# Optimization experiments

Measured on AMD Instinct MI355X. Metric: run time of the kernel, lower is better.

The kernel has to match this reference:

```python
import jax, jax.numpy as jnp
import numpy as np
import math

L, D, H, HD, F, G, V, P = 15, 512, 64, 8, 2048, 128, 7, 49
B, N = 4, 256


def setup_inputs() -> dict:
    key = jax.random.key(0)
    ks = jax.random.split(key, 24)
    nrm = lambda k, shape, s=0.02: (jax.random.normal(k, shape) * s).astype(jnp.float32)
    inp = {}
    inp["atom_types"] = jax.random.randint(ks[0], (B, N), 0, V)
    inp["coords"] = jax.random.normal(ks[1], (B, N, 3)) * 3.0
    inp["pair_types"] = jax.random.randint(ks[2], (B, N, N), 0, P)
    inp["mask"] = jnp.ones((B, N), dtype=bool)
    # embeddings / pair encoding params
    inp["atom_emb"] = nrm(ks[3], (V, D), 1.0).at[0].set(0.0)  # padding_idx=0
    inp["gaussian_mu"] = jax.random.normal(ks[4], (G,))
    inp["gaussian_sigma"] = jnp.ones((G,)) * 0.1
    inp["pair_a"] = jax.random.normal(ks[5], (P,)) * 0.01
    inp["pair_b"] = jax.random.normal(ks[6], (P,)) * 0.01
    inp["pl_w"] = nrm(ks[7], (G,))
    inp["pl_b"] = jnp.zeros(())
    # stacked per-layer params (leading dim L for lax.scan)
    inp["ln1_g"] = jnp.ones((L, D)); inp["ln1_b"] = jnp.zeros((L, D))
    inp["qkv_w"] = nrm(ks[8], (L, 3 * D, D)); inp["qkv_b"] = jnp.zeros((L, 3 * D))
    inp["pp_w"] = nrm(ks[9], (L, H), 0.1); inp["pp_b"] = jnp.zeros((L, H))
    inp["out_w"] = nrm(ks[10], (L, D, D)); inp["out_b"] = jnp.zeros((L, D))
    inp["ln2_g"] = jnp.ones((L, D)); inp["ln2_b"] = jnp.zeros((L, D))
    inp["ffn_w1"] = nrm(ks[11], (L, F, D)); inp["ffn_b1"] = jnp.zeros((L, F))
    inp["ffn_w2"] = nrm(ks[12], (L, D, F)); inp["ffn_b2"] = jnp.zeros((L, D))
    # SE3 head scalar affines (Linear(1,1) twice) and energy head
    inp["se3_uw"] = jnp.array(0.5); inp["se3_ub"] = jnp.array(0.01)
    inp["se3_ww"] = jnp.array(0.5); inp["se3_wb"] = jnp.array(0.01)
    inp["en_w"] = nrm(ks[13], (D,)); inp["en_b"] = jnp.zeros(())
    return inp


def _layernorm(x, g, b):
    m = x.mean(-1, keepdims=True)
    v = ((x - m) ** 2).mean(-1, keepdims=True)
    return (x - m) / jnp.sqrt(v + 1e-5) * g + b


def reference(atom_types, coords, pair_types, mask,
              atom_emb, gaussian_mu, gaussian_sigma, pair_a, pair_b, pl_w, pl_b,
              ln1_g, ln1_b, qkv_w, qkv_b, pp_w, pp_b, out_w, out_b,
              ln2_g, ln2_b, ffn_w1, ffn_b1, ffn_w2, ffn_b2,
              se3_uw, se3_ub, se3_ww, se3_wb, en_w, en_b):
    b_, n_ = atom_types.shape
    h = atom_emb[atom_types]  # [B,N,D]

    delta = coords[:, :, None, :] - coords[:, None, :, :]  # [B,N,N,3]
    d2 = (delta ** 2).sum(-1)
    dist = jnp.sqrt(jnp.maximum(d2, 1e-12))  # safe norm (grad-safe at 0)
    dist = jnp.where(mask[:, :, None], dist, 0.0)
    da = (pair_a[pair_types] * dist + pair_b[pair_types])[..., None]  # [B,N,N,1]
    gt = jnp.exp(-(da - gaussian_mu) ** 2) / (2.0 * gaussian_sigma ** 2)
    gt = gt / (gaussian_sigma * math.sqrt(2.0 * math.pi))
    gt = gt * mask[:, :, None, None]  # [B,N,N,G]
    pair_repr = gt @ pl_w + pl_b  # [B,N,N]
    pair_mask = mask[:, :, None] & mask[:, None, :]
    pair_repr = pair_repr * pair_mask

    scale = 1.0 / math.sqrt(HD)
    row_mask = mask[:, None, :, None]  # masks query rows, per original code

    def layer(hc, p):
        (l1g, l1b, qw, qb, ppw, ppb, ow, ob, l2g, l2b, w1, b1, w2, b2) = p
        x = _layernorm(hc, l1g, l1b)
        qkv = (x @ qw.T + qb).reshape(b_, n_, 3, H, HD)
        q, k, v = qkv[:, :, 0], qkv[:, :, 1], qkv[:, :, 2]
        scores = jnp.einsum('bnhd,bmhd->bhnm', q, k) * scale
        bias = pair_repr[..., None] * ppw + ppb  # [B,N,N,H]
        scores = scores + bias.transpose(0, 3, 1, 2)
        scores = jnp.where(row_mask, scores, -1e9)
        probs = jax.nn.softmax(scores, axis=-1)
        probs = jnp.where(jnp.isnan(probs), 0.0, probs)
        attn = jnp.einsum('bhnm,bmhd->bnhd', probs, v).reshape(b_, n_, D)
        hc = hc + attn @ ow.T + ob
        x2 = _layernorm(hc, l2g, l2b)
        ffn = jax.nn.gelu(x2 @ w1.T + b1, approximate=False) @ w2.T + b2
        return hc + ffn, None

    h, _ = jax.lax.scan(layer, h, (ln1_g, ln1_b, qkv_w, qkv_b, pp_w, pp_b,
                                   out_w, out_b, ln2_g, ln2_b,
                                   ffn_w1, ffn_b1, ffn_w2, ffn_b2))

    # --- SE3 equivariant head ---
    c = jax.nn.relu(pair_repr)[..., None]  # [B,N,N,1]
    c = c * se3_uw + se3_ub
    c = c * se3_ww + se3_wb
    c = c * mask[:, :, None, None]
    update = (delta * c).sum(axis=2)  # [B,N,3]
    num_valid = mask.sum(-1).astype(coords.dtype)[:, None, None] + 1e-6
    pred_coords = coords + update / num_valid

    cls = h[:, 0, :]
    pred_energy = cls @ en_w + en_b  # [B]
    return pred_coords, pred_energy


if __name__ == '__main__':
    out = reference(**setup_inputs())
    print(out[0].shape, out[1].shape)
```

## Files before the change

kernel.cpp:

```cpp
#include <hip/hip_runtime.h>
#include <hip/hip_bf16.h>
#include <math.h>

#define LAY 15
#define DIM 512
#define NH 64
#define HD 8
#define FF 2048
#define NG 128
#define BATCH 4
#define NTOK 256
#define PSTRIDE 524288

typedef __attribute__((ext_vector_type(8))) short short8;
typedef __attribute__((ext_vector_type(4))) short short4v;
typedef __attribute__((ext_vector_type(8))) __bf16 bf16x8;
typedef __attribute__((ext_vector_type(4))) float f32x4;

__device__ inline short f2bs(float f) {
  __bf16 b = (__bf16)f;
  return __builtin_bit_cast(short, b);
}

__global__ __launch_bounds__(256) void embed_kernel(
    const int* __restrict__ types, const float* __restrict__ emb,
    float* __restrict__ h)
{
  int idx = blockIdx.x * 256 + threadIdx.x;
  int token = idx >> 9;
  int d = idx & 511;
  h[idx] = emb[types[token] * DIM + d];
}

__global__ __launch_bounds__(256) void cvt2_kernel(
    const float* __restrict__ qkvw, const float* __restrict__ outw,
    const float* __restrict__ w1, const float* __restrict__ w2,
    short* __restrict__ dst, int basePair)
{
  size_t i = ((size_t)basePair + blockIdx.x * 256 + threadIdx.x) * 2;
  const float* src; size_t off;
  if (i < 1474560)      { src = qkvw; off = i; }
  else if (i < 1966080) { src = outw; off = i - 1474560; }
  else if (i < 3932160) { src = w1;   off = i - 1966080; }
  else                  { src = w2;   off = i - 3932160; }
  const float4* sp = (const float4*)(src + off * 8);
  float4 a = sp[0], b = sp[1], c = sp[2], d = sp[3];
  bf16x8 v0, v1;
  v0[0] = (__bf16)a.x; v0[1] = (__bf16)a.y; v0[2] = (__bf16)a.z; v0[3] = (__bf16)a.w;
  v0[4] = (__bf16)b.x; v0[5] = (__bf16)b.y; v0[6] = (__bf16)b.z; v0[7] = (__bf16)b.w;
  v1[0] = (__bf16)c.x; v1[1] = (__bf16)c.y; v1[2] = (__bf16)c.z; v1[3] = (__bf16)c.w;
  v1[4] = (__bf16)d.x; v1[5] = (__bf16)d.y; v1[6] = (__bf16)d.z; v1[7] = (__bf16)d.w;
  *(short8*)(dst + i * 8) = __builtin_bit_cast(short8, v0);
  *(short8*)(dst + i * 8 + 8) = __builtin_bit_cast(short8, v1);
}

__global__ __launch_bounds__(256) void pair_kernel(
    const int* __restrict__ pair_types, const float* __restrict__ coords,
    const float* __restrict__ mu, const float* __restrict__ sigma,
    const float* __restrict__ pa, const float* __restrict__ pb,
    const float* __restrict__ plw, const float* __restrict__ plb,
    float* __restrict__ pair_repr)
{
  __shared__ float smu[NG], sw[NG];
  int tid = threadIdx.x;
  if (tid < NG) {
    float sg = sigma[tid];
    smu[tid] = mu[tid];
    sw[tid] = plw[tid] / (2.0f * sg * sg * sg * 2.5066282746310002f);
  }
  __syncthreads();
  int idx = blockIdx.x * 256 + tid;
  int b = idx >> 16;
  int ij = idx & 65535;
  int i = ij >> 8, j = ij & 255;
  const float* ci = coords + (b * NTOK + i) * 3;
  const float* cj = coords + (b * NTOK + j) * 3;
  float dx = ci[0] - cj[0], dy = ci[1] - cj[1], dz = ci[2] - cj[2];
  float d2 = dx * dx + dy * dy + dz * dz;
  float dist = sqrtf(fmaxf(d2, 1e-12f));
  int pt = pair_types[idx];
  float da = pa[pt] * dist + pb[pt];
  float acc = 0.0f;
#pragma unroll 8
  for (int g = 0; g < NG; ++g) {
    float t = da - smu[g];
    acc += __expf(-t * t) * sw[g];
  }
  pair_repr[idx] = acc + plb[0];
}

__global__ __launch_bounds__(256) void pairT_kernel(
    const float* __restrict__ pr, float* __restrict__ prT)
{
  __shared__ float tile[32][33];
  int b = blockIdx.z;
  int i0 = blockIdx.y * 32, j0 = blockIdx.x * 32;
  int tx = threadIdx.x & 31, ty = threadIdx.x >> 5;
#pragma unroll
  for (int r = 0; r < 4; ++r)
    tile[ty + r * 8][tx] = pr[((size_t)(b * NTOK + i0 + ty + r * 8)) * NTOK + j0 + tx];
  __syncthreads();
#pragma unroll
  for (int r = 0; r < 4; ++r)
    prT[((size_t)(b * NTOK + j0 + ty + r * 8)) * NTOK + i0 + tx] = tile[tx][ty + r * 8];
}

__global__ __launch_bounds__(256) void coord_kernel(
    const float* __restrict__ coords, const float* __restrict__ pair_repr,
    const float* __restrict__ uw, const float* __restrict__ ub,
    const float* __restrict__ ww, const float* __restrict__ wb,
    float* __restrict__ out)
{
  int bi = blockIdx.x;
  int b = bi >> 8;
  int j = threadIdx.x;
  float pr = pair_repr[bi * 256 + j];
  float c = fmaxf(pr, 0.0f);
  c = c * uw[0] + ub[0];
  c = c * ww[0] + wb[0];
  const float* ci = coords + bi * 3;
  const float* cj = coords + (b * NTOK + j) * 3;
  float sx = (ci[0] - cj[0]) * c;
  float sy = (ci[1] - cj[1]) * c;
  float sz = (ci[2] - cj[2]) * c;
#pragma unroll
  for (int o = 32; o > 0; o >>= 1) {
    sx += __shfl_xor(sx, o);
    sy += __shfl_xor(sy, o);
    sz += __shfl_xor(sz, o);
  }
  __shared__ float sm[4][3];
  if ((j & 63) == 0) {
    sm[j >> 6][0] = sx; sm[j >> 6][1] = sy; sm[j >> 6][2] = sz;
  }
  __syncthreads();
  if (j < 3) {
    float u = sm[0][j] + sm[1][j] + sm[2][j] + sm[3][j];
    out[bi * 3 + j] = coords[bi * 3 + j] + u * (1.0f / (256.0f + 1e-6f));
  }
}

__global__ __launch_bounds__(256) void ln_kernel(
    const float* __restrict__ h, const float* __restrict__ g,
    const float* __restrict__ beta, short* __restrict__ x)
{
  int t = blockIdx.x;
  int tid = threadIdx.x;
  const float* hp = h + t * DIM;
  float v0 = hp[tid], v1 = hp[tid + 256];
  __shared__ float sm[4];
  float s = v0 + v1;
#pragma unroll
  for (int o = 32; o > 0; o >>= 1) s += __shfl_xor(s, o);
  if ((tid & 63) == 0) sm[tid >> 6] = s;
  __syncthreads();
  float mean = (sm[0] + sm[1] + sm[2] + sm[3]) * (1.0f / 512.0f);
  float d0 = v0 - mean, d1 = v1 - mean;
  float ss = d0 * d0 + d1 * d1;
#pragma unroll
  for (int o = 32; o > 0; o >>= 1) ss += __shfl_xor(ss, o);
  __syncthreads();
  if ((tid & 63) == 0) sm[tid >> 6] = ss;
  __syncthreads();
  float var = (sm[0] + sm[1] + sm[2] + sm[3]) * (1.0f / 512.0f);
  float rstd = rsqrtf(var + 1e-5f);
  x[t * DIM + tid] = f2bs(d0 * rstd * g[tid] + beta[tid]);
  x[t * DIM + tid + 256] = f2bs(d1 * rstd * g[tid + 256] + beta[tid + 256]);
}

__global__ __launch_bounds__(256) void ln_res_kernel(
    float* __restrict__ h, const float* __restrict__ part, int kparts,
    const float* __restrict__ g, const float* __restrict__ beta,
    short* __restrict__ x)
{
  int t = blockIdx.x;
  int tid = threadIdx.x;
  size_t base = (size_t)t * DIM;
  float v0 = h[base + tid], v1 = h[base + tid + 256];
  for (int z = 0; z < kparts; ++z) {
    v0 += part[(size_t)z * PSTRIDE + base + tid];
    v1 += part[(size_t)z * PSTRIDE + base + tid + 256];
  }
  h[base + tid] = v0;
  h[base + tid + 256] = v1;
  __shared__ float sm[4];
  float s = v0 + v1;
#pragma unroll
  for (int o = 32; o > 0; o >>= 1) s += __shfl_xor(s, o);
  if ((tid & 63) == 0) sm[tid >> 6] = s;
  __syncthreads();
  float mean = (sm[0] + sm[1] + sm[2] + sm[3]) * (1.0f / 512.0f);
  float d0 = v0 - mean, d1 = v1 - mean;
  float ss = d0 * d0 + d1 * d1;
#pragma unroll
  for (int o = 32; o > 0; o >>= 1) ss += __shfl_xor(ss, o);
  __syncthreads();
  if ((tid & 63) == 0) sm[tid >> 6] = ss;
  __syncthreads();
  float var = (sm[0] + sm[1] + sm[2] + sm[3]) * (1.0f / 512.0f);
  float rstd = rsqrtf(var + 1e-5f);
  x[base + tid] = f2bs(d0 * rstd * g[tid] + beta[tid]);
  x[base + tid + 256] = f2bs(d1 * rstd * g[tid + 256] + beta[tid + 256]);
}

template <int MODE>
__global__ __launch_bounds__(128) void mm3(
    const short* __restrict__ A, const short* __restrict__ W,
    const float* __restrict__ bias, float* __restrict__ Cf,
    short* __restrict__ Cb, int N, int K, int kparts)
{
  __shared__ short As[2][2048];
  __shared__ short Bs[2][4096];
  int tid = threadIdx.x;
  int lane = tid & 63, wv = tid >> 6;
  int fr = lane & 15, fq = lane >> 4;
  int m0 = blockIdx.y * 32, n0 = blockIdx.x * 64;
  int Ksub = K / kparts;
  int kbeg = blockIdx.z * Ksub, kend = kbeg + Ksub;

  int arow[2], acol[2], brow[4], bcol[4];
#pragma unroll
  for (int r = 0; r < 2; ++r) {
    int id = r * 128 + tid;
    arow[r] = id >> 3;
    acol[r] = (id & 7) ^ (arow[r] & 7);
  }
#pragma unroll
  for (int r = 0; r < 4; ++r) {
    int id = r * 128 + tid;
    brow[r] = id >> 3;
    bcol[r] = (id & 7) ^ (brow[r] & 7);
  }

  auto stage = [&](int p, int k0) {
#pragma unroll
    for (int r = 0; r < 2; ++r) {
      const short* ga = &A[(size_t)(m0 + arow[r]) * K + k0 + acol[r] * 8];
      __builtin_amdgcn_global_load_lds(
          (const __attribute__((address_space(1))) void*)ga,
          (__attribute__((address_space(3))) void*)&As[p][(r * 128 + wv * 64) * 8],
          16, 0, 0);
    }
#pragma unroll
    for (int r = 0; r < 4; ++r) {
      const short* gw = &W[(size_t)(n0 + brow[r]) * K + k0 + bcol[r] * 8];
      __builtin_amdgcn_global_load_lds(
          (const __attribute__((address_space(1))) void*)gw,
          (__attribute__((address_space(3))) void*)&Bs[p][(r * 128 + wv * 64) * 8],
          16, 0, 0);
    }
  };

  f32x4 acc[2][2];
#pragma unroll
  for (int i = 0; i < 2; ++i)
#pragma unroll
    for (int j = 0; j < 2; ++j) acc[i][j] = (f32x4){0.f, 0.f, 0.f, 0.f};

  int aslot[2][2], bslot[2][2];
#pragma unroll
  for (int s = 0; s < 2; ++s)
#pragma unroll
    for (int i = 0; i < 2; ++i) {
      int m = i * 16 + fr;
      int c = s * 4 + fq;
      aslot[s][i] = m * 8 + (c ^ (m & 7));
      int n = wv * 32 + i * 16 + fr;
      bslot[s][i] = n * 8 + (c ^ (n & 7));
    }

  stage(0, kbeg);
  __syncthreads();
  int p = 0;
  for (int k0 = kbeg; k0 < kend; k0 += 64) {
    if (k0 + 64 < kend) stage(p ^ 1, k0 + 64);
    short8 af[2][2], bf_[2][2];
#pragma unroll
    for (int s = 0; s < 2; ++s)
#pragma unroll
      for (int i = 0; i < 2; ++i) {
        af[s][i] = *(const short8*)&As[p][aslot[s][i] * 8];
        bf_[s][i] = *(const short8*)&Bs[p][bslot[s][i] * 8];
      }
#pragma unroll
    for (int s = 0; s < 2; ++s)
#pragma unroll
      for (int i = 0; i < 2; ++i)
#pragma unroll
        for (int j = 0; j < 2; ++j)
          acc[i][j] = __builtin_amdgcn_mfma_f32_16x16x32_bf16(
              af[s][i], bf_[s][j], acc[i][j], 0, 0, 0);
    __syncthreads();
    p ^= 1;
  }

#pragma unroll
  for (int i = 0; i < 2; ++i) {
#pragma unroll
    for (int j = 0; j < 2; ++j) {
      int col = n0 + wv * 32 + j * 16 + fr;
      float bcol = bias[col];
#pragma unroll
      for (int rr = 0; rr < 4; ++rr) {
        int row = m0 + i * 16 + fq * 4 + rr;
        size_t idx = (size_t)row * N + col;
        float v = acc[i][j][rr];
        if (MODE == 2) {
          v += bcol;
          Cb[idx] = f2bs(0.5f * v * (1.0f + erff(v * 0.70710678118654752f)));
        } else if (MODE == 3) {
          Cb[idx] = f2bs(v + bcol);
        } else {
          if (blockIdx.z == 0) v += bcol;
          Cf[(size_t)blockIdx.z * PSTRIDE + idx] = v;
        }
      }
    }
  }
}

__global__ __launch_bounds__(128) void attn_mfma(
    const short* __restrict__ qkv, const float* __restrict__ prT,
    const float* __restrict__ ppw, const float* __restrict__ ppb,
    short* __restrict__ attn)
{
  __shared__ alignas(16) short Kl[256 * 8];
  __shared__ alignas(16) short Ql[128 * 8];
  __shared__ alignas(16) short VT[8 * 264];
  __shared__ alignas(16) short P[2 * 16 * 264];
  __shared__ alignas(16) float linv[32];
  int h = blockIdx.x, b = blockIdx.y;
  int qbase = blockIdx.z * 128;
  int tid = threadIdx.x;

#pragma unroll
  for (int r0 = 0; r0 < 2; ++r0) {
    int r = tid + r0 * 128;
    short8 kv = *(const short8*)&qkv[(size_t)(b * NTOK + r) * 1536 + 512 + h * 8];
    *(short8*)&Kl[r * 8] = kv;
    short8 vv = *(const short8*)&qkv[(size_t)(b * NTOK + r) * 1536 + 1024 + h * 8];
#pragma unroll
    for (int d = 0; d < 8; ++d) VT[d * 264 + r] = vv[d];
  }
  {
    short8 qv = *(const short8*)&qkv[(size_t)(b * NTOK + qbase + tid) * 1536 + h * 8];
    *(short8*)&Ql[tid * 8] = qv;
  }
  __syncthreads();

  int lane = tid & 63, w = tid >> 6;
  int fr = lane & 15, quad = lane >> 4;
  float pw = ppw[h], pbb = ppb[h];
  const float scale = 0.35355339059327373f;
  short8 zero8 = {0, 0, 0, 0, 0, 0, 0, 0};

  short8 vfrag[8];
#pragma unroll
  for (int kc = 0; kc < 8; ++kc)
    vfrag[kc] = (fr < 8) ? *(const short8*)&VT[fr * 264 + kc * 32 + quad * 8]
                         : zero8;

  short* Pw = &P[w * 16 * 264];
  float* lw = &linv[w * 16];

  for (int qt = 0; qt < 4; ++qt) {
    int qloc = w * 64 + qt * 16;
    int qg = qbase + qloc + fr;
    const float* prp = &prT[(size_t)b * 65536 + qg];
    float prv[16][4];
#pragma unroll
    for (int t = 0; t < 16; ++t)
#pragma unroll
      for (int r = 0; r < 4; ++r)
        prv[t][r] = prp[(size_t)(t * 16 + quad * 4 + r) * NTOK];

    short8 qf = zero8;
    if (quad == 0) qf = *(const short8*)&Ql[(qloc + fr) * 8];
    f32x4 sacc[16];
#pragma unroll
    for (int t = 0; t < 16; ++t) {
      short8 kf = zero8;
      if (quad == 0) kf = *(const short8*)&Kl[(t * 16 + fr) * 8];
      sacc[t] = __builtin_amdgcn_mfma_f32_16x16x32_bf16(
          kf, qf, (f32x4){0.f, 0.f, 0.f, 0.f}, 0, 0, 0);
    }

    float l = 0.f;
#pragma unroll
    for (int t = 0; t < 16; ++t) {
      short4v pk;
#pragma unroll
      for (int r = 0; r < 4; ++r) {
        float s = sacc[t][r] * scale + prv[t][r] * pw + pbb;
        float p = __expf(s);
        l += p;
        pk[r] = f2bs(p);
      }
      *(short4v*)&Pw[fr * 264 + t * 16 + quad * 4] = pk;
    }
    l += __shfl_xor(l, 16);
    l += __shfl_xor(l, 32);
    if (lane < 16) lw[fr] = 1.0f / l;

    f32x4 oacc = (f32x4){0.f, 0.f, 0.f, 0.f};
#pragma unroll
    for (int kc = 0; kc < 8; ++kc) {
      short8 pf = *(const short8*)&Pw[fr * 264 + kc * 32 + quad * 8];
      oacc = __builtin_amdgcn_mfma_f32_16x16x32_bf16(pf, vfrag[kc], oacc, 0, 0, 0);
    }
    if (fr < 8) {
      f32x4 li = *(f32x4*)&lw[quad * 4];
#pragma unroll
      for (int r = 0; r < 4; ++r) {
        int q = qbase + qloc + quad * 4 + r;
        attn[(size_t)(b * NTOK + q) * DIM + h * 8 + fr] = f2bs(oacc[r] * li[r]);
      }
    }
  }
}

__global__ __launch_bounds__(256) void energy_kernel(
    const float* __restrict__ h, const float* __restrict__ part,
    const float* __restrict__ enw, const float* __restrict__ enb,
    float* __restrict__ out)
{
  int b = blockIdx.x;
  int tid = threadIdx.x;
  size_t base = (size_t)(b * NTOK) * DIM;
  float x0 = h[base + tid], x1 = h[base + tid + 256];
#pragma unroll
  for (int z = 0; z < 4; ++z) {
    x0 += part[(size_t)z * PSTRIDE + base + tid];
    x1 += part[(size_t)z * PSTRIDE + base + tid + 256];
  }
  float s = x0 * enw[tid] + x1 * enw[tid + 256];
  __shared__ float sm[4];
#pragma unroll
  for (int o = 32; o > 0; o >>= 1) s += __shfl_xor(s, o);
  if ((tid & 63) == 0) sm[tid >> 6] = s;
  __syncthreads();
  if (tid == 0) out[BATCH * NTOK * 3 + b] = sm[0] + sm[1] + sm[2] + sm[3] + enb[0];
}

extern "C" void kernel_launch(void* const* d_in, const int* in_sizes, int n_in,
                              void* d_out, int out_size, void* d_ws, size_t ws_size,
                              hipStream_t stream)
{
  const int*   atom_types = (const int*)d_in[0];
  const float* coords     = (const float*)d_in[1];
  const int*   pair_types = (const int*)d_in[2];
  const float* atom_emb = (const float*)d_in[4];
  const float* gmu  = (const float*)d_in[5];
  const float* gsig = (const float*)d_in[6];
  const float* pa   = (const float*)d_in[7];
  const float* pb   = (const float*)d_in[8];
  const float* plw  = (const float*)d_in[9];
  const float* plb  = (const float*)d_in[10];
  const float* ln1g = (const float*)d_in[11];
  const float* ln1b = (const float*)d_in[12];
  const float* qkvw = (const float*)d_in[13];
  const float* qkvb = (const float*)d_in[14];
  const float* ppw  = (const float*)d_in[15];
  const float* ppb  = (const float*)d_in[16];
  const float* outw = (const float*)d_in[17];
  const float* outb = (const float*)d_in[18];
  const float* ln2g = (const float*)d_in[19];
  const float* ln2b = (const float*)d_in[20];
  const float* w1   = (const float*)d_in[21];
  const float* b1   = (const float*)d_in[22];
  const float* w2   = (const float*)d_in[23];
  const float* b2   = (const float*)d_in[24];
  const float* uw   = (const float*)d_in[25];
  const float* ub   = (const float*)d_in[26];
  const float* sww  = (const float*)d_in[27];
  const float* swb  = (const float*)d_in[28];
  const float* enw  = (const float*)d_in[29];
  const float* enb  = (const float*)d_in[30];

  float* out = (float*)d_out;
  float* ws  = (float*)d_ws;
  float* pair_repr = ws;
  float* prT  = pair_repr + 262144;
  float* h    = prT + 262144;
  float* part = h + 524288;
  short* qkv_bf  = (short*)(part + 4 * 524288);
  short* x_bf    = qkv_bf + 1572864;
  short* attn_bf = x_bf + 524288;
  short* ffn1_bf = attn_bf + 524288;
  short* qkvw_bf = ffn1_bf + 2097152;
  short* outw_bf = qkvw_bf + 11796480;
  short* w1_bf   = outw_bf + 3932160;
  short* w2_bf   = w1_bf + 15728640;

  for (int c = 0; c < 8; ++c)
    cvt2_kernel<<<1440, 256, 0, stream>>>(qkvw, outw, w1, w2, qkvw_bf,
                                          c * 368640);

  embed_kernel<<<2048, 256, 0, stream>>>(atom_types, atom_emb, h);
  pair_kernel<<<1024, 256, 0, stream>>>(pair_types, coords, gmu, gsig, pa, pb,
                                        plw, plb, pair_repr);
  pairT_kernel<<<dim3(8, 8, 4), 256, 0, stream>>>(pair_repr, prT);
  coord_kernel<<<1024, 256, 0, stream>>>(coords, pair_repr, uw, ub, sww, swb, out);

  for (int l = 0; l < LAY; ++l) {
    if (l == 0)
      ln_kernel<<<1024, 256, 0, stream>>>(h, ln1g, ln1b, x_bf);
    else
      ln_res_kernel<<<1024, 256, 0, stream>>>(h, part, 4,
                                              ln1g + l * DIM, ln1b + l * DIM, x_bf);
    mm3<3><<<dim3(24, 32, 1), 128, 0, stream>>>(
        x_bf, qkvw_bf + (size_t)l * 1536 * DIM, qkvb + l * 1536, nullptr, qkv_bf,
        1536, DIM, 1);
    attn_mfma<<<dim3(NH, BATCH, 2), 128, 0, stream>>>(
        qkv_bf, prT, ppw + l * NH, ppb + l * NH, attn_bf);
    mm3<4><<<dim3(8, 32, 2), 128, 0, stream>>>(
        attn_bf, outw_bf + (size_t)l * DIM * DIM, outb + l * DIM, part, nullptr,
        DIM, DIM, 2);
    ln_res_kernel<<<1024, 256, 0, stream>>>(h, part, 2,
                                            ln2g + l * DIM, ln2b + l * DIM, x_bf);
    mm3<2><<<dim3(32, 32, 1), 128, 0, stream>>>(
        x_bf, w1_bf + (size_t)l * FF * DIM, b1 + l * FF, nullptr, ffn1_bf,
        FF, DIM, 1);
    mm3<4><<<dim3(8, 32, 4), 128, 0, stream>>>(
        ffn1_bf, w2_bf + (size_t)l * DIM * FF, b2 + l * DIM, part, nullptr,
        DIM, FF, 4);
  }
  energy_kernel<<<BATCH, 256, 0, stream>>>(h, part, enw, enb, out);
}
```

Before: 1.206 ms.

## Widen GEMM N-tile to 128, fuse coord head into pair kernel, vectorize layernorms

```diff
diff --git a/kernel.cpp b/kernel.cpp
--- a/kernel.cpp
+++ b/kernel.cpp
@@ -14,6 +14,7 @@
 
 typedef __attribute__((ext_vector_type(8))) short short8;
 typedef __attribute__((ext_vector_type(4))) short short4v;
+typedef __attribute__((ext_vector_type(2))) short short2v;
 typedef __attribute__((ext_vector_type(8))) __bf16 bf16x8;
 typedef __attribute__((ext_vector_type(4))) float f32x4;
 
@@ -59,9 +60,12 @@
     const float* __restrict__ mu, const float* __restrict__ sigma,
     const float* __restrict__ pa, const float* __restrict__ pb,
     const float* __restrict__ plw, const float* __restrict__ plb,
-    float* __restrict__ pair_repr)
+    const float* __restrict__ uw, const float* __restrict__ ub,
+    const float* __restrict__ ww, const float* __restrict__ wb,
+    float* __restrict__ pair_repr, float* __restrict__ out)
 {
   __shared__ float smu[NG], sw[NG];
+  __shared__ float sm[4][3];
   int tid = threadIdx.x;
   if (tid < NG) {
     float sg = sigma[tid];
@@ -69,11 +73,11 @@
     sw[tid] = plw[tid] / (2.0f * sg * sg * sg * 2.5066282746310002f);
   }
   __syncthreads();
-  int idx = blockIdx.x * 256 + tid;
-  int b = idx >> 16;
-  int ij = idx & 65535;
-  int i = ij >> 8, j = ij & 255;
-  const float* ci = coords + (b * NTOK + i) * 3;
+  int bi = blockIdx.x;
+  int b = bi >> 8;
+  int j = tid;
+  int idx = bi * 256 + j;
+  const float* ci = coords + bi * 3;
   const float* cj = coords + (b * NTOK + j) * 3;
   float dx = ci[0] - cj[0], dy = ci[1] - cj[1], dz = ci[2] - cj[2];
   float d2 = dx * dx + dy * dy + dz * dz;
@@ -86,7 +90,27 @@
     float t = da - smu[g];
     acc += __expf(-t * t) * sw[g];
   }
-  pair_repr[idx] = acc + plb[0];
+  float pr = acc + plb[0];
+  pair_repr[idx] = pr;
+
+  float c = fmaxf(pr, 0.0f);
+  c = c * uw[0] + ub[0];
+  c = c * ww[0] + wb[0];
+  float sx = dx * c, sy = dy * c, sz = dz * c;
+#pragma unroll
+  for (int o = 32; o > 0; o >>= 1) {
+    sx += __shfl_xor(sx, o);
+    sy += __shfl_xor(sy, o);
+    sz += __shfl_xor(sz, o);
+  }
+  if ((j & 63) == 0) {
+    sm[j >> 6][0] = sx; sm[j >> 6][1] = sy; sm[j >> 6][2] = sz;
+  }
+  __syncthreads();
+  if (j < 3) {
+    float u = sm[0][j] + sm[1][j] + sm[2][j] + sm[3][j];
+    out[bi * 3 + j] = coords[bi * 3 + j] + u * (1.0f / (256.0f + 1e-6f));
+  }
 }
 
 __global__ __launch_bounds__(256) void pairT_kernel(
@@ -105,57 +129,21 @@
     prT[((size_t)(b * NTOK + j0 + ty + r * 8)) * NTOK + i0 + tx] = tile[tx][ty + r * 8];
 }
 
-__global__ __launch_bounds__(256) void coord_kernel(
-    const float* __restrict__ coords, const float* __restrict__ pair_repr,
-    const float* __restrict__ uw, const float* __restrict__ ub,
-    const float* __restrict__ ww, const float* __restrict__ wb,
-    float* __restrict__ out)
-{
-  int bi = blockIdx.x;
-  int b = bi >> 8;
-  int j = threadIdx.x;
-  float pr = pair_repr[bi * 256 + j];
-  float c = fmaxf(pr, 0.0f);
-  c = c * uw[0] + ub[0];
-  c = c * ww[0] + wb[0];
-  const float* ci = coords + bi * 3;
-  const float* cj = coords + (b * NTOK + j) * 3;
-  float sx = (ci[0] - cj[0]) * c;
-  float sy = (ci[1] - cj[1]) * c;
-  float sz = (ci[2] - cj[2]) * c;
-#pragma unroll
-  for (int o = 32; o > 0; o >>= 1) {
-    sx += __shfl_xor(sx, o);
-    sy += __shfl_xor(sy, o);
-    sz += __shfl_xor(sz, o);
-  }
-  __shared__ float sm[4][3];
-  if ((j & 63) == 0) {
-    sm[j >> 6][0] = sx; sm[j >> 6][1] = sy; sm[j >> 6][2] = sz;
-  }
-  __syncthreads();
-  if (j < 3) {
-    float u = sm[0][j] + sm[1][j] + sm[2][j] + sm[3][j];
-    out[bi * 3 + j] = coords[bi * 3 + j] + u * (1.0f / (256.0f + 1e-6f));
-  }
-}
-
 __global__ __launch_bounds__(256) void ln_kernel(
     const float* __restrict__ h, const float* __restrict__ g,
     const float* __restrict__ beta, short* __restrict__ x)
 {
   int t = blockIdx.x;
   int tid = threadIdx.x;
-  const float* hp = h + t * DIM;
-  float v0 = hp[tid], v1 = hp[tid + 256];
+  float2 v = *(const float2*)&h[(size_t)t * DIM + tid * 2];
   __shared__ float sm[4];
-  float s = v0 + v1;
+  float s = v.x + v.y;
 #pragma unroll
   for (int o = 32; o > 0; o >>= 1) s += __shfl_xor(s, o);
   if ((tid & 63) == 0) sm[tid >> 6] = s;
   __syncthreads();
   float mean = (sm[0] + sm[1] + sm[2] + sm[3]) * (1.0f / 512.0f);
-  float d0 = v0 - mean, d1 = v1 - mean;
+  float d0 = v.x - mean, d1 = v.y - mean;
   float ss = d0 * d0 + d1 * d1;
 #pragma unroll
   for (int o = 32; o > 0; o >>= 1) ss += __shfl_xor(ss, o);
@@ -164,8 +152,12 @@
   __syncthreads();
   float var = (sm[0] + sm[1] + sm[2] + sm[3]) * (1.0f / 512.0f);
   float rstd = rsqrtf(var + 1e-5f);
-  x[t * DIM + tid] = f2bs(d0 * rstd * g[tid] + beta[tid]);
-  x[t * DIM + tid + 256] = f2bs(d1 * rstd * g[tid + 256] + beta[tid + 256]);
+  float2 gg = *(const float2*)&g[tid * 2];
+  float2 bb = *(const float2*)&beta[tid * 2];
+  short2v o2;
+  o2[0] = f2bs(d0 * rstd * gg.x + bb.x);
+  o2[1] = f2bs(d1 * rstd * gg.y + bb.y);
+  *(short2v*)&x[(size_t)t * DIM + tid * 2] = o2;
 }
 
 __global__ __launch_bounds__(256) void ln_res_kernel(
@@ -175,22 +167,21 @@
 {
   int t = blockIdx.x;
   int tid = threadIdx.x;
-  size_t base = (size_t)t * DIM;
-  float v0 = h[base + tid], v1 = h[base + tid + 256];
+  size_t base = (size_t)t * DIM + tid * 2;
+  float2 v = *(const float2*)&h[base];
   for (int z = 0; z < kparts; ++z) {
-    v0 += part[(size_t)z * PSTRIDE + base + tid];
-    v1 += part[(size_t)z * PSTRIDE + base + tid + 256];
-  }
-  h[base + tid] = v0;
-  h[base + tid + 256] = v1;
+    float2 pz = *(const float2*)&part[(size_t)z * PSTRIDE + base];
+    v.x += pz.x; v.y += pz.y;
+  }
+  *(float2*)&h[base] = v;
   __shared__ float sm[4];
-  float s = v0 + v1;
+  float s = v.x + v.y;
 #pragma unroll
   for (int o = 32; o > 0; o >>= 1) s += __shfl_xor(s, o);
   if ((tid & 63) == 0) sm[tid >> 6] = s;
   __syncthreads();
   float mean = (sm[0] + sm[1] + sm[2] + sm[3]) * (1.0f / 512.0f);
-  float d0 = v0 - mean, d1 = v1 - mean;
+  float d0 = v.x - mean, d1 = v.y - mean;
   float ss = d0 * d0 + d1 * d1;
 #pragma unroll
   for (int o = 32; o > 0; o >>= 1) ss += __shfl_xor(ss, o);
@@ -199,8 +190,12 @@
   __syncthreads();
   float var = (sm[0] + sm[1] + sm[2] + sm[3]) * (1.0f / 512.0f);
   float rstd = rsqrtf(var + 1e-5f);
-  x[base + tid] = f2bs(d0 * rstd * g[tid] + beta[tid]);
-  x[base + tid + 256] = f2bs(d1 * rstd * g[tid + 256] + beta[tid + 256]);
+  float2 gg = *(const float2*)&g[tid * 2];
+  float2 bb = *(const float2*)&beta[tid * 2];
+  short2v o2;
+  o2[0] = f2bs(d0 * rstd * gg.x + bb.x);
+  o2[1] = f2bs(d1 * rstd * gg.y + bb.y);
+  *(short2v*)&x[base] = o2;
 }
 
 template <int MODE>
@@ -210,15 +205,15 @@
     short* __restrict__ Cb, int N, int K, int kparts)
 {
   __shared__ short As[2][2048];
-  __shared__ short Bs[2][4096];
+  __shared__ short Bs[2][8192];
   int tid = threadIdx.x;
   int lane = tid & 63, wv = tid >> 6;
   int fr = lane & 15, fq = lane >> 4;
-  int m0 = blockIdx.y * 32, n0 = blockIdx.x * 64;
+  int m0 = blockIdx.y * 32, n0 = blockIdx.x * 128;
   int Ksub = K / kparts;
   int kbeg = blockIdx.z * Ksub, kend = kbeg + Ksub;
 
-  int arow[2], acol[2], brow[4], bcol[4];
+  int arow[2], acol[2], brow[8], bcol[8];
 #pragma unroll
   for (int r = 0; r < 2; ++r) {
     int id = r * 128 + tid;
@@ -226,7 +221,7 @@
     acol[r] = (id & 7) ^ (arow[r] & 7);
   }
 #pragma unroll
-  for (int r = 0; r < 4; ++r) {
+  for (int r = 0; r < 8; ++r) {
     int id = r * 128 + tid;
     brow[r] = id >> 3;
     bcol[r] = (id & 7) ^ (brow[r] & 7);
@@ -242,7 +237,7 @@
           16, 0, 0);
     }
 #pragma unroll
-    for (int r = 0; r < 4; ++r) {
+    for (int r = 0; r < 8; ++r) {
       const short* gw = &W[(size_t)(n0 + brow[r]) * K + k0 + bcol[r] * 8];
       __builtin_amdgcn_global_load_lds(
           (const __attribute__((address_space(1))) void*)gw,
@@ -251,43 +246,49 @@
     }
   };
 
-  f32x4 acc[2][2];
+  f32x4 acc[2][4];
 #pragma unroll
   for (int i = 0; i < 2; ++i)
 #pragma unroll
-    for (int j = 0; j < 2; ++j) acc[i][j] = (f32x4){0.f, 0.f, 0.f, 0.f};
-
-  int aslot[2][2], bslot[2][2];
-#pragma unroll
-  for (int s = 0; s < 2; ++s)
+    for (int j = 0; j < 4; ++j) acc[i][j] = (f32x4){0.f, 0.f, 0.f, 0.f};
+
+  int aslot[2][2], bslot[2][4];
+#pragma unroll
+  for (int s = 0; s < 2; ++s) {
+    int c = s * 4 + fq;
 #pragma unroll
     for (int i = 0; i < 2; ++i) {
       int m = i * 16 + fr;
-      int c = s * 4 + fq;
       aslot[s][i] = m * 8 + (c ^ (m & 7));
-      int n = wv * 32 + i * 16 + fr;
-      bslot[s][i] = n * 8 + (c ^ (n & 7));
-    }
+    }
+#pragma unroll
+    for (int j = 0; j < 4; ++j) {
+      int n = wv * 64 + j * 16 + fr;
+      bslot[s][j] = n * 8 + (c ^ (n & 7));
+    }
+  }
 
   stage(0, kbeg);
   __syncthreads();
   int p = 0;
   for (int k0 = kbeg; k0 < kend; k0 += 64) {
     if (k0 + 64 < kend) stage(p ^ 1, k0 + 64);
-    short8 af[2][2], bf_[2][2];
+    short8 af[2][2], bf_[2][4];
+#pragma unroll
+    for (int s = 0; s < 2; ++s) {
+#pragma unroll
+      for (int i = 0; i < 2; ++i)
+        af[s][i] = *(const short8*)&As[p][aslot[s][i] * 8];
+#pragma unroll
+      for (int j = 0; j < 4; ++j)
+        bf_[s][j] = *(const short8*)&Bs[p][bslot[s][j] * 8];
+    }
 #pragma unroll
     for (int s = 0; s < 2; ++s)
 #pragma unroll
-      for (int i = 0; i < 2; ++i) {
-        af[s][i] = *(const short8*)&As[p][aslot[s][i] * 8];
-        bf_[s][i] = *(const short8*)&Bs[p][bslot[s][i] * 8];
-      }
-#pragma unroll
-    for (int s = 0; s < 2; ++s)
-#pragma unroll
       for (int i = 0; i < 2; ++i)
 #pragma unroll
-        for (int j = 0; j < 2; ++j)
+        for (int j = 0; j < 4; ++j)
           acc[i][j] = __builtin_amdgcn_mfma_f32_16x16x32_bf16(
               af[s][i], bf_[s][j], acc[i][j], 0, 0, 0);
     __syncthreads();
@@ -297,8 +298,8 @@
 #pragma unroll
   for (int i = 0; i < 2; ++i) {
 #pragma unroll
-    for (int j = 0; j < 2; ++j) {
-      int col = n0 + wv * 32 + j * 16 + fr;
+    for (int j = 0; j < 4; ++j) {
+      int col = n0 + wv * 64 + j * 16 + fr;
       float bcol = bias[col];
 #pragma unroll
       for (int rr = 0; rr < 4; ++rr) {
@@ -492,15 +493,13 @@
   short* w1_bf   = outw_bf + 3932160;
   short* w2_bf   = w1_bf + 15728640;
 
-  for (int c = 0; c < 8; ++c)
-    cvt2_kernel<<<1440, 256, 0, stream>>>(qkvw, outw, w1, w2, qkvw_bf,
-                                          c * 368640);
+  cvt2_kernel<<<11520, 256, 0, stream>>>(qkvw, outw, w1, w2, qkvw_bf, 0);
 
   embed_kernel<<<2048, 256, 0, stream>>>(atom_types, atom_emb, h);
   pair_kernel<<<1024, 256, 0, stream>>>(pair_types, coords, gmu, gsig, pa, pb,
-                                        plw, plb, pair_repr);
+                                        plw, plb, uw, ub, sww, swb,
+                                        pair_repr, out);
   pairT_kernel<<<dim3(8, 8, 4), 256, 0, stream>>>(pair_repr, prT);
-  coord_kernel<<<1024, 256, 0, stream>>>(coords, pair_repr, uw, ub, sww, swb, out);
 
   for (int l = 0; l < LAY; ++l) {
     if (l == 0)
@@ -508,20 +507,20 @@
     else
       ln_res_kernel<<<1024, 256, 0, stream>>>(h, part, 4,
                                               ln1g + l * DIM, ln1b + l * DIM, x_bf);
-    mm3<3><<<dim3(24, 32, 1), 128, 0, stream>>>(
+    mm3<3><<<dim3(12, 32, 1), 128, 0, stream>>>(
         x_bf, qkvw_bf + (size_t)l * 1536 * DIM, qkvb + l * 1536, nullptr, qkv_bf,
         1536, DIM, 1);
     attn_mfma<<<dim3(NH, BATCH, 2), 128, 0, stream>>>(
         qkv_bf, prT, ppw + l * NH, ppb + l * NH, attn_bf);
-    mm3<4><<<dim3(8, 32, 2), 128, 0, stream>>>(
+    mm3<4><<<dim3(4, 32, 2), 128, 0, stream>>>(
         attn_bf, outw_bf + (size_t)l * DIM * DIM, outb + l * DIM, part, nullptr,
         DIM, DIM, 2);
     ln_res_kernel<<<1024, 256, 0, stream>>>(h, part, 2,
                                             ln2g + l * DIM, ln2b + l * DIM, x_bf);
-    mm3<2><<<dim3(32, 32, 1), 128, 0, stream>>>(
+    mm3<2><<<dim3(16, 32, 1), 128, 0, stream>>>(
         x_bf, w1_bf + (size_t)l * FF * DIM, b1 + l * FF, nullptr, ffn1_bf,
         FF, DIM, 1);
-    mm3<4><<<dim3(8, 32, 4), 128, 0, stream>>>(
+    mm3<4><<<dim3(4, 32, 4), 128, 0, stream>>>(
         ffn1_bf, w2_bf + (size_t)l * DIM * FF, b2 + l * DIM, part, nullptr,
         DIM, FF, 4);
   }
```

Result: slower. 1.246 ms (+3.3%).
